# Optimization experiments

Measured on AMD Instinct MI355X. Metric: run time of the kernel, lower is better.

Reference implementation:

```python
import jax, jax.numpy as jnp
import numpy as np

N = 50000        # nodes
DEG = 16         # in-degree per node
E = N * DEG      # edges
IN_F, HID, NCLS = 128, 128, 64
B, L = 1024, 50  # sentence batch, sentence length


def _linear_init(key, fan_in, fan_out):
    s = 1.0 / np.sqrt(fan_in)
    kw, kb = jax.random.split(key)
    W = jax.random.uniform(kw, (fan_in, fan_out), jnp.float32, -s, s)
    b = jax.random.uniform(kb, (fan_out,), jnp.float32, -s, s)
    return W, b


def setup_inputs() -> dict:
    key = jax.random.key(0)
    ks = jax.random.split(key, 9)
    inputs = jax.random.normal(ks[0], (N, IN_F), jnp.float32)
    src = jax.random.randint(ks[1], (E,), 0, N, dtype=jnp.int32)
    # every node has exactly DEG incoming edges -> DGL recv on all nodes is well-defined
    dst = jnp.repeat(jnp.arange(N, dtype=jnp.int32), DEG)
    sentence = jax.random.randint(ks[2], (B, L), 0, N, dtype=jnp.int32)
    W1, b1 = _linear_init(ks[3], IN_F, HID)
    W2, b2 = _linear_init(ks[4], HID, NCLS)
    Wf1, bf1 = _linear_init(ks[5], NCLS, 256)
    Wf2, bf2 = _linear_init(ks[6], 256, 128)
    Wf3, bf3 = _linear_init(ks[7], 128, 2)
    return {"inputs": inputs, "W1": W1, "b1": b1, "W2": W2, "b2": b2,
            "Wf1": Wf1, "bf1": bf1, "Wf2": Wf2, "bf2": bf2, "Wf3": Wf3, "bf3": bf3,
            "src": src, "dst": dst, "sentence": sentence}


def reference(inputs, W1, b1, W2, b2, Wf1, bf1, Wf2, bf2, Wf3, bf3, src, dst, sentence):
    def mean_agg(h):
        # gather src features, segment-mean over destinations (gcn_message/gcn_reduce)
        s = jax.ops.segment_sum(h[src], dst, num_segments=N)       # [N, d]
        cnt = jax.ops.segment_sum(jnp.ones((E, 1), h.dtype), dst, num_segments=N)
        return s / jnp.maximum(cnt, 1.0)

    x = jax.nn.relu(mean_agg(inputs) @ W1 + b1)   # gc1 + relu (dropout = identity, eval mode)
    x = mean_agg(x) @ W2 + b2                      # gc2
    x = x.at[0].set(0.0)                           # x[0] = zeros
    sent_emd = jnp.sum(x[sentence], axis=1)        # [B, NCLS]
    h1 = jax.nn.relu(sent_emd @ Wf1 + bf1)
    h2 = jax.nn.relu(h1 @ Wf2 + bf2)
    return h2 @ Wf3 + bf3                          # [B, 2]
```

## Files before the change

### kernel.cpp

```cpp
#include <hip/hip_runtime.h>

#define NNODES 50000
#define DEG    16
#define NCLS   64
#define BSENT  1024
#define LSENT  50

typedef __attribute__((ext_vector_type(8))) short short8;
typedef __attribute__((ext_vector_type(4))) float f32x4;

__device__ __forceinline__ unsigned short f2bf(float f) {
    union { float f; unsigned u; } v; v.f = f;
    unsigned r = v.u + 0x7fffu + ((v.u >> 16) & 1u);
    return (unsigned short)(r >> 16);
}

__device__ __forceinline__ void prep_one(const float* W, unsigned short* Bp,
                                         int idx, int NOUT) {
    int j    = idx & 7;
    int lane = (idx >> 3) & 63;
    int rem  = idx >> 9;
    int ks   = rem & 3, c = rem >> 2;
    int k = ks * 32 + (lane >> 4) * 8 + j;
    int n = c * 16 + (lane & 15);
    Bp[idx] = f2bf(W[k * NOUT + n]);
}

__global__ void prep_both(const float* __restrict__ W1, unsigned short* __restrict__ B1p,
                          const float* __restrict__ W2, unsigned short* __restrict__ B2p) {
    int idx = blockIdx.x * 256 + threadIdx.x;
    if (idx < 128 * 128)            prep_one(W1, B1p, idx, 128);
    else if (idx < 128 * 128 + 64 * 128) prep_one(W2, B2p, idx - 128 * 128, 64);
}

__global__ __launch_bounds__(256)
void gemm_mfma1(const float* __restrict__ X, const unsigned short* __restrict__ Bp,
                unsigned short* __restrict__ Y, int M) {
    __shared__ __align__(16) unsigned short As[64 * 128];
    __shared__ __align__(16) unsigned short Bs[128 * 128];
    const int tid  = threadIdx.x;
    const int wave = tid >> 6, lane = tid & 63;
    const int mbase = blockIdx.x * 64;

#pragma unroll
    for (int i = 0; i < 8; ++i) {
        int idx = tid + i * 256;
        int row = idx >> 5;
        int c4  = idx & 31;
        int grow = mbase + row;
        int w  = row >> 4;
        int ks = c4 >> 3;
        int ln = ((c4 >> 1) & 3) * 16 + (row & 15);
        int off = ((w * 4 + ks) * 64 + ln) * 8 + (c4 & 1) * 4;
        unsigned lo = 0, hi = 0;
        if (grow < M) {
            const float4 v = *(const float4*)&X[(size_t)grow * 128 + c4 * 4];
            lo = (unsigned)f2bf(v.x) | ((unsigned)f2bf(v.y) << 16);
            hi = (unsigned)f2bf(v.z) | ((unsigned)f2bf(v.w) << 16);
        }
        *(uint2*)&As[off] = make_uint2(lo, hi);
    }
#pragma unroll
    for (int i = 0; i < 8; ++i) {
        int idx = tid + i * 256;
        *(uint4*)&Bs[idx * 8] = *(const uint4*)&Bp[idx * 8];
    }
    __syncthreads();

    const short8* Af = (const short8*)As;
    const short8* Bf = (const short8*)Bs;
    short8 a[4];
#pragma unroll
    for (int ks = 0; ks < 4; ++ks) a[ks] = Af[(wave * 4 + ks) * 64 + lane];

    f32x4 acc[8] = {};
#pragma unroll
    for (int c = 0; c < 8; ++c)
#pragma unroll
        for (int ks = 0; ks < 4; ++ks)
            acc[c] = __builtin_amdgcn_mfma_f32_16x16x32_bf16(
                a[ks], Bf[(c * 4 + ks) * 64 + lane], acc[c], 0, 0, 0);

    const int col = lane & 15, rg = lane >> 4;
#pragma unroll
    for (int c = 0; c < 8; ++c)
#pragma unroll
        for (int r = 0; r < 4; ++r) {
            int grow = mbase + wave * 16 + rg * 4 + r;
            if (grow < M) Y[(size_t)grow * 128 + c * 16 + col] = f2bf(acc[c][r]);
        }
}

__global__ __launch_bounds__(256)
void agg_gemm(const unsigned short* __restrict__ Y1, const int* __restrict__ src,
              const float* __restrict__ b1, const unsigned short* __restrict__ B2p,
              unsigned short* __restrict__ Y2, int M) {
    __shared__ __align__(16) unsigned short As[64 * 128];
    __shared__ __align__(16) unsigned short Bs[64 * 128];
    __shared__ int s_idx[64 * DEG];
    const int tid  = threadIdx.x;
    const int wave = tid >> 6, lane = tid & 63;
    const int mbase = blockIdx.x * 64;
    const long eb = (long)mbase * DEG;

    for (int e = tid; e < 64 * DEG; e += 256)
        s_idx[e] = (eb + e < (long)NNODES * DEG) ? src[eb + e] : 0;
#pragma unroll
    for (int i = 0; i < 4; ++i) {
        int idx = tid + i * 256;
        *(uint4*)&Bs[idx * 8] = *(const uint4*)&B2p[idx * 8];
    }
    __syncthreads();

#pragma unroll
    for (int i = 0; i < 8; ++i) {
        int slot = tid + i * 256;
        int row = slot >> 5, c4 = slot & 31;
        int grow = mbase + row;
        float a0 = 0.f, a1 = 0.f, a2 = 0.f, a3 = 0.f;
        if (grow < M) {
            const int* sp = &s_idx[row * DEG];
#pragma unroll
            for (int j = 0; j < DEG; ++j) {
                const uint2 v = *(const uint2*)&Y1[(size_t)sp[j] * 128 + c4 * 4];
                a0 += __uint_as_float(v.x << 16);
                a1 += __uint_as_float(v.x & 0xffff0000u);
                a2 += __uint_as_float(v.y << 16);
                a3 += __uint_as_float(v.y & 0xffff0000u);
            }
            const float s = 1.f / 16.f;
            const float4 bb = *(const float4*)&b1[c4 * 4];
            a0 = fmaxf(a0 * s + bb.x, 0.f);
            a1 = fmaxf(a1 * s + bb.y, 0.f);
            a2 = fmaxf(a2 * s + bb.z, 0.f);
            a3 = fmaxf(a3 * s + bb.w, 0.f);
        }
        int w  = row >> 4;
        int ks = c4 >> 3;
        int ln = ((c4 >> 1) & 3) * 16 + (row & 15);
        int off = ((w * 4 + ks) * 64 + ln) * 8 + (c4 & 1) * 4;
        unsigned lo = (unsigned)f2bf(a0) | ((unsigned)f2bf(a1) << 16);
        unsigned hi = (unsigned)f2bf(a2) | ((unsigned)f2bf(a3) << 16);
        *(uint2*)&As[off] = make_uint2(lo, hi);
    }
    __syncthreads();

    const short8* Af = (const short8*)As;
    const short8* Bf = (const short8*)Bs;
    short8 a[4];
#pragma unroll
    for (int ks = 0; ks < 4; ++ks) a[ks] = Af[(wave * 4 + ks) * 64 + lane];

    f32x4 acc[4] = {};
#pragma unroll
    for (int c = 0; c < 4; ++c)
#pragma unroll
        for (int ks = 0; ks < 4; ++ks)
            acc[c] = __builtin_amdgcn_mfma_f32_16x16x32_bf16(
                a[ks], Bf[(c * 4 + ks) * 64 + lane], acc[c], 0, 0, 0);

    const int col = lane & 15, rg = lane >> 4;
#pragma unroll
    for (int c = 0; c < 4; ++c)
#pragma unroll
        for (int r = 0; r < 4; ++r) {
            int grow = mbase + wave * 16 + rg * 4 + r;
            if (grow < M) Y2[(size_t)grow * 64 + c * 16 + col] = f2bf(acc[c][r]);
        }
}

__global__ __launch_bounds__(256)
void agg2(const unsigned short* __restrict__ Y, const int* __restrict__ src,
          const float* __restrict__ bias, float* __restrict__ out) {
    constexpr int TPN = 16, NPB = 16;
    __shared__ int s_idx[NPB * DEG];
    const int tid = threadIdx.x;
    const int nb = blockIdx.x * NPB;
    if (tid < NPB * DEG) s_idx[tid] = src[nb * DEG + tid];
    __syncthreads();
    const int ln = tid / TPN;
    const int c  = tid % TPN;
    const int n  = nb + ln;
    const int* sp = &s_idx[ln * DEG];
    float a0 = 0.f, a1 = 0.f, a2 = 0.f, a3 = 0.f;
#pragma unroll
    for (int j = 0; j < DEG; ++j) {
        const uint2 v = *(const uint2*)&Y[(size_t)sp[j] * 64 + c * 4];
        a0 += __uint_as_float(v.x << 16);
        a1 += __uint_as_float(v.x & 0xffff0000u);
        a2 += __uint_as_float(v.y << 16);
        a3 += __uint_as_float(v.y & 0xffff0000u);
    }
    const float s = 1.f / 16.f;
    a0 = a0 * s + bias[c * 4 + 0];
    a1 = a1 * s + bias[c * 4 + 1];
    a2 = a2 * s + bias[c * 4 + 2];
    a3 = a3 * s + bias[c * 4 + 3];
    if (n == 0) { a0 = a1 = a2 = a3 = 0.f; }
    *(float4*)&out[(size_t)n * 64 + c * 4] = make_float4(a0, a1, a2, a3);
}

__global__ __launch_bounds__(256)
void head_fused(const float* __restrict__ x2, const int* __restrict__ sentence,
                const float* __restrict__ Wf1, const float* __restrict__ bf1,
                const float* __restrict__ Wf2, const float* __restrict__ bf2,
                const float* __restrict__ Wf3, const float* __restrict__ bf3,
                float* __restrict__ out) {
    __shared__ int   s_idx[8 * LSENT];
    __shared__ float sent_s[8][64];
    __shared__ float h1_s[8][256];
    __shared__ float h2_s[8][128];
    const int tid = threadIdx.x;
    const int bs = blockIdx.x * 8;

    for (int e = tid; e < 8 * LSENT; e += 256)
        s_idx[e] = sentence[bs * LSENT + e];
    __syncthreads();

    {
        const int s = tid >> 5, l32 = tid & 31;
        float c0 = 0.f, c1 = 0.f;
        const int* sp = &s_idx[s * LSENT];
#pragma unroll 5
        for (int l = 0; l < LSENT; ++l) {
            const float2 v = *(const float2*)&x2[(size_t)sp[l] * 64 + l32 * 2];
            c0 += v.x; c1 += v.y;
        }
        sent_s[s][l32 * 2 + 0] = c0;
        sent_s[s][l32 * 2 + 1] = c1;
    }
    __syncthreads();

    {
        const int s = tid >> 5, og = (tid & 31) * 8;
        float acc[8];
#pragma unroll
        for (int j = 0; j < 8; ++j) acc[j] = bf1[og + j];
        for (int k = 0; k < 64; ++k) {
            const float xk = sent_s[s][k];
            const float4 w0 = *(const float4*)&Wf1[k * 256 + og];
            const float4 w1 = *(const float4*)&Wf1[k * 256 + og + 4];
            acc[0] += xk * w0.x; acc[1] += xk * w0.y; acc[2] += xk * w0.z; acc[3] += xk * w0.w;
            acc[4] += xk * w1.x; acc[5] += xk * w1.y; acc[6] += xk * w1.z; acc[7] += xk * w1.w;
        }
#pragma unroll
        for (int j = 0; j < 8; ++j) h1_s[s][og + j] = fmaxf(acc[j], 0.f);
    }
    __syncthreads();

    {
        const int s = tid >> 5, og = (tid & 31) * 4;
        float acc[4];
#pragma unroll
        for (int j = 0; j < 4; ++j) acc[j] = bf2[og + j];
        for (int k = 0; k < 256; ++k) {
            const float xk = h1_s[s][k];
            const float4 w = *(const float4*)&Wf2[k * 128 + og];
            acc[0] += xk * w.x; acc[1] += xk * w.y; acc[2] += xk * w.z; acc[3] += xk * w.w;
        }
#pragma unroll
        for (int j = 0; j < 4; ++j) h2_s[s][og + j] = fmaxf(acc[j], 0.f);
    }
    __syncthreads();

    if (tid < 16) {
        const int s = tid >> 1, c = tid & 1;
        float acc = bf3[c];
        for (int k = 0; k < 128; ++k)
            acc += h2_s[s][k] * Wf3[k * 2 + c];
        out[(bs + s) * 2 + c] = acc;
    }
}

extern "C" void kernel_launch(void* const* d_in, const int* in_sizes, int n_in,
                              void* d_out, int out_size, void* d_ws, size_t ws_size,
                              hipStream_t stream) {
    const float* inputs  = (const float*)d_in[0];
    const float* W1      = (const float*)d_in[1];
    const float* b1      = (const float*)d_in[2];
    const float* W2      = (const float*)d_in[3];
    const float* b2      = (const float*)d_in[4];
    const float* Wf1     = (const float*)d_in[5];
    const float* bf1     = (const float*)d_in[6];
    const float* Wf2     = (const float*)d_in[7];
    const float* bf2     = (const float*)d_in[8];
    const float* Wf3     = (const float*)d_in[9];
    const float* bf3     = (const float*)d_in[10];
    const int*   src     = (const int*)d_in[11];
    const int*   sentence= (const int*)d_in[13];
    float* out = (float*)d_out;

    char* ws = (char*)d_ws;
    size_t o = 0;
    auto alloc = [&](size_t bytes) -> char* {
        char* p = ws + o; o += (bytes + 255) & ~(size_t)255; return p;
    };
    unsigned short* Y1  = (unsigned short*)alloc((size_t)NNODES * 128 * 2);
    unsigned short* Y2  = (unsigned short*)alloc((size_t)NNODES * 64 * 2);
    float*          x2  = (float*)alloc((size_t)NNODES * 64 * 4);
    unsigned short* B1p = (unsigned short*)alloc(128 * 128 * 2);
    unsigned short* B2p = (unsigned short*)alloc(64 * 128 * 2);

    const int gridM = (NNODES + 63) / 64;

    prep_both<<<(128 * 128 + 64 * 128 + 255) / 256, 256, 0, stream>>>(W1, B1p, W2, B2p);
    gemm_mfma1<<<gridM, 256, 0, stream>>>(inputs, B1p, Y1, NNODES);
    agg_gemm<<<gridM, 256, 0, stream>>>(Y1, src, b1, B2p, Y2, NNODES);
    agg2<<<NNODES / 16, 256, 0, stream>>>(Y2, src, b2, x2);
    head_fused<<<BSENT / 8, 256, 0, stream>>>(x2, sentence, Wf1, bf1, Wf2, bf2, Wf3, bf3, out);
}
```

Before: 86.10 us.

## Split fused aggregate+GEMM into feature-sliced gather kernels and separate GEMM

Replaces the fused agg_gemm kernel with a standalone feature-sliced gather kernel that writes a bf16 intermediate x1, followed by a templated MFMA GEMM. The gather is launched as slices over feature columns (32 features per slice, 32 nodes per block), so concurrently running blocks touch a narrower column band of the table, which is meant to improve cache locality of the random gathers. The second aggregation uses the same sliced scheme. This costs an extra kernel launch plus a full write and reread of the 50000x128 bf16 intermediate.

```diff
diff --git a/kernel.cpp b/kernel.cpp
--- a/kernel.cpp
+++ b/kernel.cpp
@@ -5,6 +5,7 @@
 #define NCLS   64
 #define BSENT  1024
 #define LSENT  50
+#define NCHUNK 1563
 
 typedef __attribute__((ext_vector_type(8))) short short8;
 typedef __attribute__((ext_vector_type(4))) float f32x4;
@@ -13,6 +14,9 @@
     union { float f; unsigned u; } v; v.f = f;
     unsigned r = v.u + 0x7fffu + ((v.u >> 16) & 1u);
     return (unsigned short)(r >> 16);
+}
+__device__ __forceinline__ unsigned pack2bf(float a, float b) {
+    return (unsigned)f2bf(a) | ((unsigned)f2bf(b) << 16);
 }
 
 __device__ __forceinline__ void prep_one(const float* W, unsigned short* Bp,
@@ -29,15 +33,16 @@
 __global__ void prep_both(const float* __restrict__ W1, unsigned short* __restrict__ B1p,
                           const float* __restrict__ W2, unsigned short* __restrict__ B2p) {
     int idx = blockIdx.x * 256 + threadIdx.x;
-    if (idx < 128 * 128)            prep_one(W1, B1p, idx, 128);
+    if (idx < 128 * 128)                 prep_one(W1, B1p, idx, 128);
     else if (idx < 128 * 128 + 64 * 128) prep_one(W2, B2p, idx - 128 * 128, 64);
 }
 
+template<int A_BF16, int NOUT>
 __global__ __launch_bounds__(256)
-void gemm_mfma1(const float* __restrict__ X, const unsigned short* __restrict__ Bp,
-                unsigned short* __restrict__ Y, int M) {
+void gemm_mfma(const void* __restrict__ Xv, const unsigned short* __restrict__ Bp,
+               unsigned short* __restrict__ Y, int M) {
     __shared__ __align__(16) unsigned short As[64 * 128];
-    __shared__ __align__(16) unsigned short Bs[128 * 128];
+    __shared__ __align__(16) unsigned short Bs[NOUT * 128];
     const int tid  = threadIdx.x;
     const int wave = tid >> 6, lane = tid & 63;
     const int mbase = blockIdx.x * 64;
@@ -54,14 +59,19 @@
         int off = ((w * 4 + ks) * 64 + ln) * 8 + (c4 & 1) * 4;
         unsigned lo = 0, hi = 0;
         if (grow < M) {
-            const float4 v = *(const float4*)&X[(size_t)grow * 128 + c4 * 4];
-            lo = (unsigned)f2bf(v.x) | ((unsigned)f2bf(v.y) << 16);
-            hi = (unsigned)f2bf(v.z) | ((unsigned)f2bf(v.w) << 16);
+            if (A_BF16) {
+                const uint2 v = *(const uint2*)((const unsigned short*)Xv + (size_t)grow * 128 + c4 * 4);
+                lo = v.x; hi = v.y;
+            } else {
+                const float4 v = *(const float4*)((const float*)Xv + (size_t)grow * 128 + c4 * 4);
+                lo = pack2bf(v.x, v.y);
+                hi = pack2bf(v.z, v.w);
+            }
         }
         *(uint2*)&As[off] = make_uint2(lo, hi);
     }
 #pragma unroll
-    for (int i = 0; i < 8; ++i) {
+    for (int i = 0; i < NOUT * 128 / (8 * 256); ++i) {
         int idx = tid + i * 256;
         *(uint4*)&Bs[idx * 8] = *(const uint4*)&Bp[idx * 8];
     }
@@ -73,9 +83,9 @@
 #pragma unroll
     for (int ks = 0; ks < 4; ++ks) a[ks] = Af[(wave * 4 + ks) * 64 + lane];
 
-    f32x4 acc[8] = {};
-#pragma unroll
-    for (int c = 0; c < 8; ++c)
+    f32x4 acc[NOUT / 16] = {};
+#pragma unroll
+    for (int c = 0; c < NOUT / 16; ++c)
 #pragma unroll
         for (int ks = 0; ks < 4; ++ks)
             acc[c] = __builtin_amdgcn_mfma_f32_16x16x32_bf16(
@@ -83,121 +93,66 @@
 
     const int col = lane & 15, rg = lane >> 4;
 #pragma unroll
-    for (int c = 0; c < 8; ++c)
+    for (int c = 0; c < NOUT / 16; ++c)
 #pragma unroll
         for (int r = 0; r < 4; ++r) {
             int grow = mbase + wave * 16 + rg * 4 + r;
-            if (grow < M) Y[(size_t)grow * 128 + c * 16 + col] = f2bf(acc[c][r]);
-        }
-}
-
+            if (grow < M) Y[(size_t)grow * NOUT + c * 16 + col] = f2bf(acc[c][r]);
+        }
+}
+
+template<int FTAB, int RELU, int ZERO0, int OUT_BF16>
 __global__ __launch_bounds__(256)
-void agg_gemm(const unsigned short* __restrict__ Y1, const int* __restrict__ src,
-              const float* __restrict__ b1, const unsigned short* __restrict__ B2p,
-              unsigned short* __restrict__ Y2, int M) {
-    __shared__ __align__(16) unsigned short As[64 * 128];
-    __shared__ __align__(16) unsigned short Bs[64 * 128];
-    __shared__ int s_idx[64 * DEG];
-    const int tid  = threadIdx.x;
-    const int wave = tid >> 6, lane = tid & 63;
-    const int mbase = blockIdx.x * 64;
-    const long eb = (long)mbase * DEG;
-
-    for (int e = tid; e < 64 * DEG; e += 256)
-        s_idx[e] = (eb + e < (long)NNODES * DEG) ? src[eb + e] : 0;
-#pragma unroll
-    for (int i = 0; i < 4; ++i) {
-        int idx = tid + i * 256;
-        *(uint4*)&Bs[idx * 8] = *(const uint4*)&B2p[idx * 8];
-    }
-    __syncthreads();
-
-#pragma unroll
-    for (int i = 0; i < 8; ++i) {
-        int slot = tid + i * 256;
-        int row = slot >> 5, c4 = slot & 31;
-        int grow = mbase + row;
-        float a0 = 0.f, a1 = 0.f, a2 = 0.f, a3 = 0.f;
-        if (grow < M) {
-            const int* sp = &s_idx[row * DEG];
-#pragma unroll
-            for (int j = 0; j < DEG; ++j) {
-                const uint2 v = *(const uint2*)&Y1[(size_t)sp[j] * 128 + c4 * 4];
-                a0 += __uint_as_float(v.x << 16);
-                a1 += __uint_as_float(v.x & 0xffff0000u);
-                a2 += __uint_as_float(v.y << 16);
-                a3 += __uint_as_float(v.y & 0xffff0000u);
-            }
-            const float s = 1.f / 16.f;
-            const float4 bb = *(const float4*)&b1[c4 * 4];
-            a0 = fmaxf(a0 * s + bb.x, 0.f);
-            a1 = fmaxf(a1 * s + bb.y, 0.f);
-            a2 = fmaxf(a2 * s + bb.z, 0.f);
-            a3 = fmaxf(a3 * s + bb.w, 0.f);
-        }
-        int w  = row >> 4;
-        int ks = c4 >> 3;
-        int ln = ((c4 >> 1) & 3) * 16 + (row & 15);
-        int off = ((w * 4 + ks) * 64 + ln) * 8 + (c4 & 1) * 4;
-        unsigned lo = (unsigned)f2bf(a0) | ((unsigned)f2bf(a1) << 16);
-        unsigned hi = (unsigned)f2bf(a2) | ((unsigned)f2bf(a3) << 16);
-        *(uint2*)&As[off] = make_uint2(lo, hi);
-    }
-    __syncthreads();
-
-    const short8* Af = (const short8*)As;
-    const short8* Bf = (const short8*)Bs;
-    short8 a[4];
-#pragma unroll
-    for (int ks = 0; ks < 4; ++ks) a[ks] = Af[(wave * 4 + ks) * 64 + lane];
-
-    f32x4 acc[4] = {};
-#pragma unroll
-    for (int c = 0; c < 4; ++c)
-#pragma unroll
-        for (int ks = 0; ks < 4; ++ks)
-            acc[c] = __builtin_amdgcn_mfma_f32_16x16x32_bf16(
-                a[ks], Bf[(c * 4 + ks) * 64 + lane], acc[c], 0, 0, 0);
-
-    const int col = lane & 15, rg = lane >> 4;
-#pragma unroll
-    for (int c = 0; c < 4; ++c)
-#pragma unroll
-        for (int r = 0; r < 4; ++r) {
-            int grow = mbase + wave * 16 + rg * 4 + r;
-            if (grow < M) Y2[(size_t)grow * 64 + c * 16 + col] = f2bf(acc[c][r]);
-        }
-}
-
-__global__ __launch_bounds__(256)
-void agg2(const unsigned short* __restrict__ Y, const int* __restrict__ src,
-          const float* __restrict__ bias, float* __restrict__ out) {
-    constexpr int TPN = 16, NPB = 16;
-    __shared__ int s_idx[NPB * DEG];
+void agg_slice(const unsigned short* __restrict__ T, const int* __restrict__ src,
+               const float* __restrict__ bias, void* __restrict__ outv) {
+    const int bid   = blockIdx.x;
+    const int slice = bid / NCHUNK;
+    const int chunk = bid - slice * NCHUNK;
+    const int nb    = chunk * 32;
+    __shared__ int s_idx[32 * DEG];
     const int tid = threadIdx.x;
-    const int nb = blockIdx.x * NPB;
-    if (tid < NPB * DEG) s_idx[tid] = src[nb * DEG + tid];
-    __syncthreads();
-    const int ln = tid / TPN;
-    const int c  = tid % TPN;
-    const int n  = nb + ln;
-    const int* sp = &s_idx[ln * DEG];
+    {
+        const int eb = nb * DEG;
+        int e = tid;
+#pragma unroll
+        for (int i = 0; i < 2; ++i, e += 256)
+            s_idx[e] = (eb + e < NNODES * DEG) ? src[eb + e] : 0;
+    }
+    __syncthreads();
+
+    const int row = tid >> 3, part = tid & 7;
+    const int n = nb + row;
+    if (n >= NNODES) return;
+    const int fo = slice * 32 + part * 4;
+    const int* sp = &s_idx[row * DEG];
+
     float a0 = 0.f, a1 = 0.f, a2 = 0.f, a3 = 0.f;
 #pragma unroll
     for (int j = 0; j < DEG; ++j) {
-        const uint2 v = *(const uint2*)&Y[(size_t)sp[j] * 64 + c * 4];
+        const uint2 v = *(const uint2*)&T[(size_t)sp[j] * FTAB + fo];
         a0 += __uint_as_float(v.x << 16);
         a1 += __uint_as_float(v.x & 0xffff0000u);
         a2 += __uint_as_float(v.y << 16);
         a3 += __uint_as_float(v.y & 0xffff0000u);
     }
     const float s = 1.f / 16.f;
-    a0 = a0 * s + bias[c * 4 + 0];
-    a1 = a1 * s + bias[c * 4 + 1];
-    a2 = a2 * s + bias[c * 4 + 2];
-    a3 = a3 * s + bias[c * 4 + 3];
-    if (n == 0) { a0 = a1 = a2 = a3 = 0.f; }
-    *(float4*)&out[(size_t)n * 64 + c * 4] = make_float4(a0, a1, a2, a3);
+    const float4 bb = *(const float4*)&bias[fo];
+    a0 = a0 * s + bb.x;
+    a1 = a1 * s + bb.y;
+    a2 = a2 * s + bb.z;
+    a3 = a3 * s + bb.w;
+    if (RELU) {
+        a0 = fmaxf(a0, 0.f); a1 = fmaxf(a1, 0.f);
+        a2 = fmaxf(a2, 0.f); a3 = fmaxf(a3, 0.f);
+    }
+    if (ZERO0 && n == 0) { a0 = a1 = a2 = a3 = 0.f; }
+
+    if (OUT_BF16) {
+        *(uint2*)((unsigned short*)outv + (size_t)n * FTAB + fo) =
+            make_uint2(pack2bf(a0, a1), pack2bf(a2, a3));
+    } else {
+        *(float4*)((float*)outv + (size_t)n * FTAB + fo) = make_float4(a0, a1, a2, a3);
+    }
 }
 
 __global__ __launch_bounds__(256)
@@ -296,6 +251,7 @@
         char* p = ws + o; o += (bytes + 255) & ~(size_t)255; return p;
     };
     unsigned short* Y1  = (unsigned short*)alloc((size_t)NNODES * 128 * 2);
+    unsigned short* x1  = (unsigned short*)alloc((size_t)NNODES * 128 * 2);
     unsigned short* Y2  = (unsigned short*)alloc((size_t)NNODES * 64 * 2);
     float*          x2  = (float*)alloc((size_t)NNODES * 64 * 4);
     unsigned short* B1p = (unsigned short*)alloc(128 * 128 * 2);
@@ -304,8 +260,9 @@
     const int gridM = (NNODES + 63) / 64;
 
     prep_both<<<(128 * 128 + 64 * 128 + 255) / 256, 256, 0, stream>>>(W1, B1p, W2, B2p);
-    gemm_mfma1<<<gridM, 256, 0, stream>>>(inputs, B1p, Y1, NNODES);
-    agg_gemm<<<gridM, 256, 0, stream>>>(Y1, src, b1, B2p, Y2, NNODES);
-    agg2<<<NNODES / 16, 256, 0, stream>>>(Y2, src, b2, x2);
+    gemm_mfma<0, 128><<<gridM, 256, 0, stream>>>(inputs, B1p, Y1, NNODES);
+    agg_slice<128, 1, 0, 1><<<NCHUNK * 4, 256, 0, stream>>>(Y1, src, b1, x1);
+    gemm_mfma<1, 64><<<gridM, 256, 0, stream>>>(x1, B2p, Y2, NNODES);
+    agg_slice<64, 0, 1, 0><<<NCHUNK * 2, 256, 0, stream>>>(Y2, src, b2, x2);
     head_fused<<<BSENT / 8, 256, 0, stream>>>(x2, sentence, Wf1, bf1, Wf2, bf2, Wf3, bf3, out);
 }
```

Measured after the change: 102.3 us. 18.9% more time.
